# Optimization experiments

Hardware: AMD Instinct MI355X
Metric: run time of the kernel (lower is better)

## Reference

```python
import jax, jax.numpy as jnp
import numpy as np

B, F, P, DM = 1, 16, 256, 1024            # batch, frames, patches, mm_hidden_size
HID = 4096                                 # config.hidden_size
DI, DSTATE, DTRANK, DCONV = 2 * DM, 16, DM // 16, 4


def _layernorm(x, w, b):
    mu = x.mean(-1, keepdims=True)
    var = ((x - mu) ** 2).mean(-1, keepdims=True)
    return (x - mu) * jax.lax.rsqrt(var + 1e-5) * w + b


def _selective_scan(u, dt, A, Bm, Cm, Dv):
    # u, dt: [b,L,d]; Bm, Cm: [b,L,n]; A: [d,n]; Dv: [d]
    def step(h, inp):
        dt_t, B_t, C_t, u_t = inp  # [b,d],[b,n],[b,n],[b,d]
        h = jnp.exp(dt_t[..., None] * A) * h + (dt_t * u_t)[..., None] * B_t[:, None, :]
        return h, jnp.einsum('bdn,bn->bd', h, C_t)
    h0 = jnp.zeros((u.shape[0], A.shape[0], A.shape[1]), u.dtype)
    _, ys = jax.lax.scan(step, h0, (jnp.swapaxes(dt, 0, 1), jnp.swapaxes(Bm, 0, 1),
                                    jnp.swapaxes(Cm, 0, 1), jnp.swapaxes(u, 0, 1)))
    return jnp.swapaxes(ys, 0, 1) + u * Dv


def _mamba_block(x, ln_w, ln_b, in_proj_w, conv_w, conv_b, x_proj_w,
                 dt_proj_w, dt_proj_b, A_log, D_param, out_proj_w):
    res = x
    x = _layernorm(x, ln_w, ln_b)
    xz = x @ in_proj_w                       # [b,L,2*DI]
    xin, z = jnp.split(xz, 2, axis=-1)
    xt = jnp.swapaxes(xin, 1, 2)             # [b,DI,L]
    xt = jax.lax.conv_general_dilated(xt, conv_w[:, None, :], (1,), [(DCONV - 1, 0)],
                                      dimension_numbers=('NCH', 'OIH', 'NCH'),
                                      feature_group_count=DI)
    xt = xt + conv_b[:, None]
    u = jax.nn.silu(jnp.swapaxes(xt, 1, 2))  # [b,L,DI]
    x_dbl = u @ x_proj_w                     # [b,L,DTRANK+2*DSTATE]
    dt_raw, Bm, Cm = jnp.split(x_dbl, [DTRANK, DTRANK + DSTATE], axis=-1)
    dt = jax.nn.softplus(dt_raw @ dt_proj_w + dt_proj_b)
    A = -jnp.exp(A_log)
    y = _selective_scan(u, dt, A, Bm, Cm, D_param)
    y = y * jax.nn.silu(z)
    return res + y @ out_proj_w


def setup_inputs() -> dict:
    key = jax.random.key(0)
    ks = jax.random.split(key, 8)
    s = 0.02
    return {
        'vst': jax.random.normal(ks[0], (B, F, P, DM), jnp.float32),
        'ln_w': jnp.ones((DM,), jnp.float32), 'ln_b': jnp.zeros((DM,), jnp.float32),
        'in_proj_w': jax.random.normal(ks[1], (DM, 2 * DI), jnp.float32) * s,
        'conv_w': jax.random.normal(ks[2], (DI, DCONV), jnp.float32) * s,
        'conv_b': jnp.zeros((DI,), jnp.float32),
        'x_proj_w': jax.random.normal(ks[3], (DI, DTRANK + 2 * DSTATE), jnp.float32) * s,
        'dt_proj_w': jax.random.normal(ks[4], (DTRANK, DI), jnp.float32) * s,
        'dt_proj_b': jnp.full((DI,), -4.6, jnp.float32),  # softplus ~ 0.01
        'A_log': jnp.log(jnp.tile(jnp.arange(1, DSTATE + 1, dtype=jnp.float32), (DI, 1))),
        'D_param': jnp.ones((DI,), jnp.float32),
        'out_proj_w': jax.random.normal(ks[5], (DI, DM), jnp.float32) * s,
        'fln_w': jnp.ones((DM,), jnp.float32), 'fln_b': jnp.zeros((DM,), jnp.float32),
        'mlp_w1': jax.random.normal(ks[6], (DM, HID), jnp.float32) * s,
        'mlp_b1': jnp.zeros((HID,), jnp.float32),
        'mlp_w2': jax.random.normal(ks[7], (HID, HID), jnp.float32) * s,
        'mlp_b2': jnp.zeros((HID,), jnp.float32),
    }


def reference(vst, ln_w, ln_b, in_proj_w, conv_w, conv_b, x_proj_w, dt_proj_w,
              dt_proj_b, A_log, D_param, out_proj_w, fln_w, fln_b,
              mlp_w1, mlp_b1, mlp_w2, mlp_b2):
    b, f, p, d = vst.shape
    h = w = int(p ** 0.5)
    # the chain of rearranges in the source is a net reshape to b (f h w) d
    x = vst.reshape(b, f * h * w, d)
    x = _mamba_block(x, ln_w, ln_b, in_proj_w, conv_w, conv_b, x_proj_w,
                     dt_proj_w, dt_proj_b, A_log, D_param, out_proj_w)
    x = _layernorm(x, fln_w, fln_b)
    # AvgPool3d kernel=(1,4,4), stride=(1,4,4) over (f,h,w)
    x = x.reshape(b, f, h // 4, 4, w // 4, 4, d).mean(axis=(3, 5))
    x = x.reshape(b, f * (h // 4) * (w // 4), d)
    y = jax.nn.gelu(x @ mlp_w1 + mlp_b1, approximate=False)
    return y @ mlp_w2 + mlp_b2
```

## Files before the change

### kernel.cpp

```cpp
#include <hip/hip_runtime.h>
#include <hip/hip_bf16.h>
#include <math.h>

typedef __hip_bfloat16 bf16_t;
typedef __attribute__((ext_vector_type(8))) short short8;
typedef __attribute__((ext_vector_type(4))) float f32x4;

#define L_SEQ   4096
#define DMODEL  1024
#define DI      2048
#define NST     16
#define DTRANK  64
#define XDBL_N  96
#define HID     4096
#define CHUNK   32
#define NCHUNK  128
#define POOLED_ROWS 256

__device__ __forceinline__ void async_load16(const bf16_t* g, bf16_t* l) {
    __builtin_amdgcn_global_load_lds(
        (const __attribute__((address_space(1))) void*)g,
        (__attribute__((address_space(3))) void*)l,
        16, 0, 0);
}
__device__ __forceinline__ void async_load16f(const float* g, float* l) {
    __builtin_amdgcn_global_load_lds(
        (const __attribute__((address_space(1))) void*)g,
        (__attribute__((address_space(3))) void*)l,
        16, 0, 0);
}

__device__ __forceinline__ float softplus_f(float x) {
    return fmaxf(x, 0.f) + __logf(1.f + __expf(-fabsf(x)));
}

__global__ __launch_bounds__(256)
void transpose_all_kernel(const float* __restrict__ j0, bf16_t* __restrict__ o0,
                          const float* __restrict__ j1, bf16_t* __restrict__ o1,
                          const float* __restrict__ j2, bf16_t* __restrict__ o2,
                          const float* __restrict__ j3, bf16_t* __restrict__ o3,
                          const float* __restrict__ j4, bf16_t* __restrict__ o4) {
    int b = blockIdx.x;
    const float* in; bf16_t* out; int K, N, Npad, local;
    if (b < 512)        { in = j0; out = o0; K = 1024; N = 4096; Npad = 4096; local = b; }
    else if (b < 544)   { in = j1; out = o1; K = 2048; N = 96;   Npad = 128;  local = b - 512; }
    else if (b < 576)   { in = j2; out = o2; K = 64;   N = 2048; Npad = 2048; local = b - 544; }
    else if (b < 832)   { in = j3; out = o3; K = 2048; N = 1024; Npad = 1024; local = b - 576; }
    else                { in = j4; out = o4; K = 1024; N = 4096; Npad = 4096; local = b - 832; }
    int nt = Npad >> 6;
    int k0 = (local / nt) << 7, n0 = (local % nt) << 6;

    __shared__ float t[64 * 129];
    int tid = threadIdx.x;
    int kkb = tid >> 4;
    int nq  = (tid & 15) * 4;
#pragma unroll
    for (int it = 0; it < 8; it++) {
        int kl = it * 16 + kkb;
        int gk = k0 + kl, gn = n0 + nq;
        float4 v = {0.f, 0.f, 0.f, 0.f};
        if (gk < K) {
            const float* src = in + (size_t)gk * N + gn;
            if (gn + 3 < N) v = *(const float4*)src;
            else {
                if (gn + 0 < N) v.x = src[0];
                if (gn + 1 < N) v.y = src[1];
                if (gn + 2 < N) v.z = src[2];
                if (gn + 3 < N) v.w = src[3];
            }
        }
        t[(nq + 0) * 129 + kl] = v.x;
        t[(nq + 1) * 129 + kl] = v.y;
        t[(nq + 2) * 129 + kl] = v.z;
        t[(nq + 3) * 129 + kl] = v.w;
    }
    __syncthreads();
#pragma unroll
    for (int it = 0; it < 4; it++) {
        int slot = it * 256 + tid;
        int nn = slot >> 4, kc = (slot & 15) * 8;
        if (k0 + kc >= K) continue;
        const float* r = &t[nn * 129 + kc];
        short8 o;
#pragma unroll
        for (int j = 0; j < 8; j++) {
            bf16_t h = __float2bfloat16(r[j]);
            o[j] = *(short*)&h;
        }
        *(short8*)(out + (size_t)(n0 + nn) * K + k0 + kc) = o;
    }
}

__global__ __launch_bounds__(256)
void ln_kernel(const float* __restrict__ x, const float* __restrict__ w,
               const float* __restrict__ b, bf16_t* __restrict__ out) {
    int row = blockIdx.x;
    int tid = threadIdx.x;
    const float* xr = x + (size_t)row * DMODEL;
    float v[4];
    float s = 0.f, ss = 0.f;
#pragma unroll
    for (int e = 0; e < 4; e++) {
        v[e] = xr[tid + e * 256];
        s += v[e];
        ss += v[e] * v[e];
    }
#pragma unroll
    for (int off = 32; off > 0; off >>= 1) {
        s  += __shfl_down(s, off);
        ss += __shfl_down(ss, off);
    }
    __shared__ float rs[4], rss[4];
    int wid = tid >> 6;
    if ((tid & 63) == 0) { rs[wid] = s; rss[wid] = ss; }
    __syncthreads();
    s  = rs[0] + rs[1] + rs[2] + rs[3];
    ss = rss[0] + rss[1] + rss[2] + rss[3];
    float mu  = s * (1.f / DMODEL);
    float var = ss * (1.f / DMODEL) - mu * mu;
    float inv = rsqrtf(var + 1e-5f);
#pragma unroll
    for (int e = 0; e < 4; e++) {
        int col = tid + e * 256;
        out[(size_t)row * DMODEL + col] =
            __float2bfloat16((v[e] - mu) * inv * w[col] + b[col]);
    }
}

__global__ __launch_bounds__(256)
void ln_pool_a_kernel(const bf16_t* __restrict__ part, size_t pstride,
                      const float* __restrict__ res, const float* __restrict__ w,
                      const float* __restrict__ b, float* __restrict__ pool_part) {
    int blk = blockIdx.x;
    int p = blk >> 2, ii = blk & 3;
    int tid = threadIdx.x;
    int f = p >> 4, i4 = (p >> 2) & 3, j4 = p & 3;
    __shared__ float rs[4], rss[4];
    float acc[4] = {0.f, 0.f, 0.f, 0.f};
    float wv[4], bv[4];
#pragma unroll
    for (int e = 0; e < 4; e++) { wv[e] = w[tid + e * 256]; bv[e] = b[tid + e * 256]; }
    for (int jj = 0; jj < 4; jj++) {
        int row = f * 256 + (i4 * 4 + ii) * 16 + j4 * 4 + jj;
        size_t ro = (size_t)row * DMODEL;
        float v[4];
        float s = 0.f, ss = 0.f;
#pragma unroll
        for (int e = 0; e < 4; e++) {
            int col = tid + e * 256;
            float x = res[ro + col]
                    + __bfloat162float(part[ro + col])
                    + __bfloat162float(part[pstride + ro + col]);
            v[e] = x;
            s += x;
            ss += x * x;
        }
#pragma unroll
        for (int off = 32; off > 0; off >>= 1) {
            s  += __shfl_down(s, off);
            ss += __shfl_down(ss, off);
        }
        int wid = tid >> 6;
        if ((tid & 63) == 0) { rs[wid] = s; rss[wid] = ss; }
        __syncthreads();
        s  = rs[0] + rs[1] + rs[2] + rs[3];
        ss = rss[0] + rss[1] + rss[2] + rss[3];
        float mu  = s * (1.f / DMODEL);
        float var = ss * (1.f / DMODEL) - mu * mu;
        float inv = rsqrtf(var + 1e-5f);
#pragma unroll
        for (int e = 0; e < 4; e++)
            acc[e] += (v[e] - mu) * inv * wv[e] + bv[e];
        __syncthreads();
    }
#pragma unroll
    for (int e = 0; e < 4; e++)
        pool_part[(size_t)blk * DMODEL + tid + e * 256] = acc[e];
}

__global__ __launch_bounds__(256)
void ln_pool_b_kernel(const float* __restrict__ pool_part, bf16_t* __restrict__ pooled) {
    int idx = blockIdx.x * 256 + threadIdx.x;
    if (idx >= POOLED_ROWS * DMODEL) return;
    int p = idx >> 10, col = idx & (DMODEL - 1);
    float s = pool_part[(size_t)(p * 4 + 0) * DMODEL + col]
            + pool_part[(size_t)(p * 4 + 1) * DMODEL + col]
            + pool_part[(size_t)(p * 4 + 2) * DMODEL + col]
            + pool_part[(size_t)(p * 4 + 3) * DMODEL + col];
    pooled[idx] = __float2bfloat16(s * (1.f / 16.f));
}

template <int EPI>
__global__ __launch_bounds__(256, 2)
void mfma_gemm(const bf16_t* __restrict__ A, int lda,
               const bf16_t* __restrict__ Bt, int ldb,
               int K,
               float* __restrict__ Cf, bf16_t* __restrict__ Cb, int ldc,
               const float* __restrict__ bias, const float* __restrict__ res) {
    __shared__ bf16_t Asl[128 * 32];
    __shared__ bf16_t Bsl[128 * 32];
    const int tid = threadIdx.x;
    const int l = tid & 63, w = tid >> 6;
    const int m0 = blockIdx.y * 128, n0 = blockIdx.x * 128;
    const int wm = (w >> 1) * 64, wn = (w & 1) * 64;

    const int srow = tid >> 2;
    const int skc = (tid & 3) * 8;
    const bf16_t* Ag = A + (size_t)(m0 + srow) * lda + skc;
    const bf16_t* Bg = Bt + (size_t)(n0 + srow) * ldb + skc;
    bf16_t* As0 = Asl + (size_t)(w * 64) * 8;
    bf16_t* As1 = Asl + (size_t)(256 + w * 64) * 8;
    bf16_t* Bs0 = Bsl + (size_t)(w * 64) * 8;
    bf16_t* Bs1 = Bsl + (size_t)(256 + w * 64) * 8;

    f32x4 acc[4][4];
#pragma unroll
    for (int i = 0; i < 4; i++)
#pragma unroll
        for (int j = 0; j < 4; j++) acc[i][j] = (f32x4){0.f, 0.f, 0.f, 0.f};

    const short8* Asv = (const short8*)Asl;
    const short8* Bsv = (const short8*)Bsl;
    const int fr = l >> 4;
    const int fc = l & 15;

    for (int k0 = 0; k0 < K; k0 += 32) {
        __syncthreads();
        async_load16(Ag, As0);
        async_load16(Ag + (size_t)64 * lda, As1);
        async_load16(Bg, Bs0);
        async_load16(Bg + (size_t)64 * ldb, Bs1);
        Ag += 32; Bg += 32;
        __syncthreads();

        short8 a[4], b[4];
#pragma unroll
        for (int im = 0; im < 4; im++)
            a[im] = Asv[(wm + im * 16 + fc) * 4 + fr];
#pragma unroll
        for (int in = 0; in < 4; in++)
            b[in] = Bsv[(wn + in * 16 + fc) * 4 + fr];
#pragma unroll
        for (int im = 0; im < 4; im++)
#pragma unroll
            for (int in = 0; in < 4; in++)
                acc[im][in] = __builtin_amdgcn_mfma_f32_16x16x32_bf16(
                    a[im], b[in], acc[im][in], 0, 0, 0);
    }

#pragma unroll
    for (int im = 0; im < 4; im++) {
        int mbase = m0 + wm + im * 16 + fr * 4;
#pragma unroll
        for (int in = 0; in < 4; in++) {
            int n = n0 + wn + in * 16 + fc;
            float bv = (EPI == 1) ? bias[n] : 0.f;
#pragma unroll
            for (int v = 0; v < 4; v++) {
                float x = acc[im][in][v];
                size_t off = (size_t)(mbase + v) * ldc + n;
                if (EPI == 0) {
                    Cb[off] = __float2bfloat16(x);
                } else if (EPI == 1) {
                    Cb[off] = __float2bfloat16(softplus_f(x + bv));
                }
            }
        }
    }
}

template <bool PBF16>
__global__ __launch_bounds__(256, 2)
void mfma_gemm_splitk(const bf16_t* __restrict__ A, int lda,
                      const bf16_t* __restrict__ Bt, int ldb,
                      int Kper, void* __restrict__ Cpart, int ldc,
                      size_t pstride) {
    __shared__ bf16_t Asl[128 * 32];
    __shared__ bf16_t Bsl[128 * 32];
    const int tid = threadIdx.x;
    const int l = tid & 63, w = tid >> 6;
    const int m0 = blockIdx.y * 128, n0 = blockIdx.x * 128;
    const int wm = (w >> 1) * 64, wn = (w & 1) * 64;
    const int kbase = blockIdx.z * Kper;

    const int srow = tid >> 2;
    const int skc = (tid & 3) * 8;
    const bf16_t* Ag = A + (size_t)(m0 + srow) * lda + kbase + skc;
    const bf16_t* Bg = Bt + (size_t)(n0 + srow) * ldb + kbase + skc;
    bf16_t* As0 = Asl + (size_t)(w * 64) * 8;
    bf16_t* As1 = Asl + (size_t)(256 + w * 64) * 8;
    bf16_t* Bs0 = Bsl + (size_t)(w * 64) * 8;
    bf16_t* Bs1 = Bsl + (size_t)(256 + w * 64) * 8;

    f32x4 acc[4][4];
#pragma unroll
    for (int i = 0; i < 4; i++)
#pragma unroll
        for (int j = 0; j < 4; j++) acc[i][j] = (f32x4){0.f, 0.f, 0.f, 0.f};

    const short8* Asv = (const short8*)Asl;
    const short8* Bsv = (const short8*)Bsl;
    const int fr = l >> 4;
    const int fc = l & 15;

    for (int k0 = 0; k0 < Kper; k0 += 32) {
        __syncthreads();
        async_load16(Ag, As0);
        async_load16(Ag + (size_t)64 * lda, As1);
        async_load16(Bg, Bs0);
        async_load16(Bg + (size_t)64 * ldb, Bs1);
        Ag += 32; Bg += 32;
        __syncthreads();

        short8 a[4], b[4];
#pragma unroll
        for (int im = 0; im < 4; im++)
            a[im] = Asv[(wm + im * 16 + fc) * 4 + fr];
#pragma unroll
        for (int in = 0; in < 4; in++)
            b[in] = Bsv[(wn + in * 16 + fc) * 4 + fr];
#pragma unroll
        for (int im = 0; im < 4; im++)
#pragma unroll
            for (int in = 0; in < 4; in++)
                acc[im][in] = __builtin_amdgcn_mfma_f32_16x16x32_bf16(
                    a[im], b[in], acc[im][in], 0, 0, 0);
    }

#pragma unroll
    for (int im = 0; im < 4; im++) {
        int mbase = m0 + wm + im * 16 + fr * 4;
#pragma unroll
        for (int in = 0; in < 4; in++) {
            int n = n0 + wn + in * 16 + fc;
#pragma unroll
            for (int v = 0; v < 4; v++) {
                size_t o = (size_t)(mbase + v) * ldc + n;
                if (PBF16)
                    ((bf16_t*)Cpart)[(size_t)blockIdx.z * pstride + o] =
                        __float2bfloat16(acc[im][in][v]);
                else
                    ((float*)Cpart)[(size_t)blockIdx.z * pstride + o] = acc[im][in][v];
            }
        }
    }
}

__global__ __launch_bounds__(512, 1)
void gemm_nt_kernel(const bf16_t* __restrict__ A, int lda,
                    const float* __restrict__ B, int ldb,
                    int Kper, float* __restrict__ Cpart, int ldc,
                    size_t pstride) {
    __shared__ bf16_t Asl[256 * 32];
    __shared__ float  Bsl[32 * 64];
    const int tid = threadIdx.x;
    const int l = tid & 63, w = tid >> 6;
    const int n0 = blockIdx.x * 64;
    const int kbase = blockIdx.z * Kper;
    const int wm = w * 32;

    const int a_row = tid >> 2, a_kc = (tid & 3) * 8;
    const bf16_t* Ag = A + (size_t)a_row * lda + kbase + a_kc;
    bf16_t* As0 = Asl + (size_t)(w * 64) * 8;
    bf16_t* As1 = Asl + (size_t)(512 + w * 64) * 8;
    const int b_row = tid >> 4, b_nc = (tid & 15) * 4;
    const float* Bg = B + (size_t)(kbase + b_row) * ldb + n0 + b_nc;
    float* Bs0 = Bsl + (size_t)(w * 64) * 4;

    f32x4 acc[2][4];
#pragma unroll
    for (int i = 0; i < 2; i++)
#pragma unroll
        for (int j = 0; j < 4; j++) acc[i][j] = (f32x4){0.f, 0.f, 0.f, 0.f};

    const short8* Asv = (const short8*)Asl;
    const int fr = l >> 4, fc = l & 15;

    for (int k0 = 0; k0 < Kper; k0 += 32) {
        __syncthreads();
        async_load16(Ag, As0);
        async_load16(Ag + (size_t)128 * lda, As1);
        async_load16f(Bg, Bs0);
        Ag += 32;
        Bg += (size_t)32 * ldb;
        __syncthreads();

        short8 a[2], bfr[4];
        a[0] = Asv[(wm + fc) * 4 + fr];
        a[1] = Asv[(wm + 16 + fc) * 4 + fr];
#pragma unroll
        for (int j = 0; j < 4; j++) {
            const float* bp = Bsl + (size_t)(fr * 8) * 64 + j * 16 + fc;
            short8 t;
#pragma unroll
            for (int i = 0; i < 8; i++) {
                bf16_t h = __float2bfloat16(bp[i * 64]);
                t[i] = *(short*)&h;
            }
            bfr[j] = t;
        }
#pragma unroll
        for (int im = 0; im < 2; im++)
#pragma unroll
            for (int j = 0; j < 4; j++)
                acc[im][j] = __builtin_amdgcn_mfma_f32_16x16x32_bf16(
                    a[im], bfr[j], acc[im][j], 0, 0, 0);
    }

    float* Cz = Cpart + (size_t)blockIdx.z * pstride;
#pragma unroll
    for (int im = 0; im < 2; im++) {
        int mbase = wm + im * 16 + fr * 4;
#pragma unroll
        for (int j = 0; j < 4; j++) {
            int n = n0 + j * 16 + fc;
#pragma unroll
            for (int v = 0; v < 4; v++)
                Cz[(size_t)(mbase + v) * ldc + n] = acc[im][j][v];
        }
    }
}

template <int S, int EPI>
__global__ __launch_bounds__(256)
void reduce_splitk4(const float* __restrict__ part, size_t pstride, int ldp,
                    int M, int N, float* __restrict__ outf, bf16_t* __restrict__ outb,
                    int ldo, const float* __restrict__ bias) {
    int idx = blockIdx.x * 256 + threadIdx.x;
    int npr = N >> 2;
    if (idx >= M * npr) return;
    int r = idx / npr, c = (idx - r * npr) << 2;
    f32x4 s = (f32x4){0.f, 0.f, 0.f, 0.f};
#pragma unroll
    for (int z = 0; z < S; z++)
        s += *(const f32x4*)(part + (size_t)z * pstride + (size_t)r * ldp + c);
    size_t o = (size_t)r * ldo + c;
    if (EPI == 0) {
        *(f32x4*)(outf + o) = s;
        short8 pk;
        ushort4 ub;
#pragma unroll
        for (int e = 0; e < 4; e++) {
            bf16_t h = __float2bfloat16(s[e]);
            ((unsigned short*)&ub)[e] = *(unsigned short*)&h;
        }
        *(ushort4*)(outb + o) = ub;
        (void)pk;
    } else if (EPI == 1) {
        f32x4 bv = *(const f32x4*)(bias + c);
        ushort4 ub;
#pragma unroll
        for (int e = 0; e < 4; e++) {
            float x = s[e] + bv[e];
            x = 0.5f * x * (1.f + erff(x * 0.70710678118654752f));
            bf16_t h = __float2bfloat16(x);
            ((unsigned short*)&ub)[e] = *(unsigned short*)&h;
        }
        *(ushort4*)(outb + o) = ub;
    } else {
        f32x4 bv = *(const f32x4*)(bias + c);
        *(f32x4*)(outf + o) = s + bv;
    }
}

__global__ __launch_bounds__(256)
void conv_silu_kernel(const bf16_t* __restrict__ xz, const float* __restrict__ cw,
                      const float* __restrict__ cb, bf16_t* __restrict__ u) {
    int idx = blockIdx.x * 256 + threadIdx.x;
    if (idx >= L_SEQ * DI / 2) return;
    int chp = idx & (DI / 2 - 1);
    int l   = idx >> 10;
    int ch  = chp * 2;
    float acc0 = cb[ch], acc1 = cb[ch + 1];
    const float4* cwv = (const float4*)(cw + ch * 4);
    float4 c0 = cwv[0], c1 = cwv[1];
    float w0[4] = {c0.x, c0.y, c0.z, c0.w};
    float w1[4] = {c1.x, c1.y, c1.z, c1.w};
#pragma unroll
    for (int k = 0; k < 4; k++) {
        int ls = l - 3 + k;
        if (ls >= 0) {
            const bf16_t* p = xz + (size_t)ls * (2 * DI) + ch;
            acc0 += w0[k] * __bfloat162float(p[0]);
            acc1 += w1[k] * __bfloat162float(p[1]);
        }
    }
    float s0 = acc0 / (1.f + __expf(-acc0));
    float s1 = acc1 / (1.f + __expf(-acc1));
    bf16_t o0 = __float2bfloat16(s0), o1 = __float2bfloat16(s1);
    unsigned int packed = (unsigned int)*(unsigned short*)&o0 |
                          ((unsigned int)*(unsigned short*)&o1 << 16);
    *(unsigned int*)(u + (size_t)l * DI + ch) = packed;
}

__global__ __launch_bounds__(256)
void scan_pass1(const bf16_t* __restrict__ dt, const bf16_t* __restrict__ u,
                const float* __restrict__ x_dbl, const float* __restrict__ A_log,
                float* __restrict__ dtsum, float* __restrict__ Sw) {
    int c = blockIdx.x;
    int tid = threadIdx.x;
    int lane = tid & 63, w = tid >> 6;
    int dloc = w * 32 + (lane & 31);
    int n0 = (lane >> 5) * 8;
    int d = blockIdx.y * 128 + dloc;
    int l0 = c * CHUNK;
    __shared__ float sB[CHUNK * NST];
    for (int i = tid; i < CHUNK * NST; i += 256)
        sB[i] = x_dbl[(size_t)(l0 + (i >> 4)) * XDBL_N + DTRANK + (i & 15)];
    __syncthreads();
    float Areg[8], h[8];
#pragma unroll
    for (int j = 0; j < 8; j++) {
        Areg[j] = -__expf(A_log[d * NST + n0 + j]);
        h[j] = 0.f;
    }
    float dts = 0.f;
    float dtl = __bfloat162float(dt[(size_t)l0 * DI + d]);
    float ul  = __bfloat162float(u[(size_t)l0 * DI + d]);
    for (int l = 0; l < CHUNK; l++) {
        float dtn = 0.f, un = 0.f;
        if (l + 1 < CHUNK) {
            int gl = l0 + l + 1;
            dtn = __bfloat162float(dt[(size_t)gl * DI + d]);
            un  = __bfloat162float(u[(size_t)gl * DI + d]);
        }
        float du = dtl * ul;
        dts += dtl;
#pragma unroll
        for (int j = 0; j < 8; j++) {
            float a = __expf(dtl * Areg[j]);
            h[j] = a * h[j] + du * sB[l * NST + n0 + j];
        }
        dtl = dtn; ul = un;
    }
    size_t base = ((size_t)c * DI + d) * NST + n0;
#pragma unroll
    for (int j = 0; j < 8; j++)
        Sw[base + j] = h[j];
    if (n0 == 0)
        dtsum[(size_t)c * DI + d] = dts;
}

__global__ __launch_bounds__(256)
void scan_pass2(const float* __restrict__ dtsum, const float* __restrict__ A_log,
                float* __restrict__ SwInit) {
    int tid = blockIdx.x * 256 + threadIdx.x;
    if (tid >= DI * NST) return;
    int d = tid >> 4;
    float A = -__expf(A_log[tid]);
    const size_t DN = DI * NST;
    float h = 0.f;
    for (int c = 0; c < NCHUNK; c += 8) {
        float ds8[8], s8[8];
#pragma unroll
        for (int j = 0; j < 8; j++) {
            ds8[j] = dtsum[(size_t)(c + j) * DI + d];
            s8[j]  = SwInit[(size_t)(c + j) * DN + tid];
        }
#pragma unroll
        for (int j = 0; j < 8; j++) {
            float p = __expf(ds8[j] * A);
            SwInit[(size_t)(c + j) * DN + tid] = h;
            h = p * h + s8[j];
        }
    }
}

__global__ __launch_bounds__(256)
void scan_pass3(const bf16_t* __restrict__ dt, const bf16_t* __restrict__ u,
                const float* __restrict__ x_dbl, const float* __restrict__ A_log,
                const float* __restrict__ Dp, const float* __restrict__ initw,
                const bf16_t* __restrict__ xz, bf16_t* __restrict__ yy) {
    int c = blockIdx.x;
    int tid = threadIdx.x;
    int lane = tid & 63, w = tid >> 6;
    int dloc = w * 32 + (lane & 31);
    int n0 = (lane >> 5) * 8;
    int d = blockIdx.y * 128 + dloc;
    int l0 = c * CHUNK;
    __shared__ float sBC[CHUNK * 2 * NST];
    for (int i = tid; i < CHUNK * 2 * NST; i += 256)
        sBC[i] = x_dbl[(size_t)(l0 + (i >> 5)) * XDBL_N + DTRANK + (i & 31)];
    __syncthreads();
    float Areg[8], h[8];
    size_t base = ((size_t)c * DI + d) * NST + n0;
#pragma unroll
    for (int j = 0; j < 8; j++) {
        Areg[j] = -__expf(A_log[d * NST + n0 + j]);
        h[j] = initw[base + j];
    }
    float Dd = Dp[d];
    float dtl = __bfloat162float(dt[(size_t)l0 * DI + d]);
    float ul  = __bfloat162float(u[(size_t)l0 * DI + d]);
    float zv  = __bfloat162float(xz[(size_t)l0 * (2 * DI) + DI + d]);
    for (int l = 0; l < CHUNK; l++) {
        float dtn = 0.f, un = 0.f, zn = 0.f;
        if (l + 1 < CHUNK) {
            int gl = l0 + l + 1;
            dtn = __bfloat162float(dt[(size_t)gl * DI + d]);
            un  = __bfloat162float(u[(size_t)gl * DI + d]);
            zn  = __bfloat162float(xz[(size_t)gl * (2 * DI) + DI + d]);
        }
        float du = dtl * ul;
        float y = 0.f;
#pragma unroll
        for (int j = 0; j < 8; j++) {
            float a = __expf(dtl * Areg[j]);
            h[j] = a * h[j] + du * sBC[l * 32 + n0 + j];
            y += h[j] * sBC[l * 32 + NST + n0 + j];
        }
        y += __shfl_xor(y, 32);
        float sz = zv / (1.f + __expf(-zv));
        if ((lane >> 5) == 0)
            yy[(size_t)(l0 + l) * DI + d] = __float2bfloat16((y + ul * Dd) * sz);
        dtl = dtn; ul = un; zv = zn;
    }
}

extern "C" void kernel_launch(void* const* d_in, const int* in_sizes, int n_in,
                              void* d_out, int out_size, void* d_ws, size_t ws_size,
                              hipStream_t stream) {
    const float* vst        = (const float*)d_in[0];
    const float* ln_w       = (const float*)d_in[1];
    const float* ln_b       = (const float*)d_in[2];
    const float* in_proj_w  = (const float*)d_in[3];
    const float* conv_w     = (const float*)d_in[4];
    const float* conv_b     = (const float*)d_in[5];
    const float* x_proj_w   = (const float*)d_in[6];
    const float* dt_proj_w  = (const float*)d_in[7];
    const float* dt_proj_b  = (const float*)d_in[8];
    const float* A_log      = (const float*)d_in[9];
    const float* D_param    = (const float*)d_in[10];
    const float* out_proj_w = (const float*)d_in[11];
    const float* fln_w      = (const float*)d_in[12];
    const float* fln_b      = (const float*)d_in[13];
    const float* mlp_w1     = (const float*)d_in[14];
    const float* mlp_b1     = (const float*)d_in[15];
    const float* mlp_w2     = (const float*)d_in[16];
    const float* mlp_b2     = (const float*)d_in[17];
    float* out = (float*)d_out;

    char* wsb = (char*)d_ws;
    size_t off = 0;
    auto alloc_bf = [&](size_t n) { bf16_t* p = (bf16_t*)(wsb + off); off += n * 2; return p; };
    auto alloc_f  = [&](size_t n) { float*  p = (float*)(wsb + off); off += n * 4; return p; };

    bf16_t* w1t  = alloc_bf((size_t)(2 * DI) * DMODEL);
    bf16_t* xpt  = alloc_bf((size_t)128 * DI);
    bf16_t* dtpt = alloc_bf((size_t)DI * DTRANK);
    bf16_t* opt  = alloc_bf((size_t)DMODEL * DI);
    bf16_t* m1t  = alloc_bf((size_t)HID * DMODEL);
    bf16_t* m2t  = alloc_bf((size_t)HID * HID);
    bf16_t* xz_bf   = alloc_bf((size_t)L_SEQ * 2 * DI);
    bf16_t* u_bf    = alloc_bf((size_t)L_SEQ * DI);
    bf16_t* dt_bf   = alloc_bf((size_t)L_SEQ * DI);
    bf16_t* xdbl_bf = alloc_bf((size_t)L_SEQ * XDBL_N);
    bf16_t* yy_bf   = alloc_bf((size_t)L_SEQ * DI);
    float*  xdbl_f  = alloc_f((size_t)L_SEQ * XDBL_N);
    float*  Pw      = alloc_f((size_t)NCHUNK * DI * NST);
    float*  Sw      = alloc_f((size_t)NCHUNK * DI * NST);
    bf16_t* xn_bf   = yy_bf;
    float*  g2part  = Pw;
    float*  dtsum   = Pw;
    bf16_t* g4part  = xz_bf;
    bf16_t* pooled  = dt_bf;
    bf16_t* h1_bf   = dt_bf + (size_t)POOLED_ROWS * DMODEL;
    float*  pool_part = (float*)yy_bf;
    float*  g5part  = (float*)yy_bf;
    float*  g6part  = (float*)m2t;

    dim3 blk256(256);

    transpose_all_kernel<<<1344, blk256, 0, stream>>>(
        in_proj_w, w1t, x_proj_w, xpt, dt_proj_w, dtpt,
        out_proj_w, opt, mlp_w1, m1t);

    ln_kernel<<<L_SEQ, blk256, 0, stream>>>(vst, ln_w, ln_b, xn_bf);

    mfma_gemm<0><<<dim3((2 * DI) / 128, L_SEQ / 128), blk256, 0, stream>>>(
        xn_bf, DMODEL, w1t, DMODEL, DMODEL, nullptr, xz_bf, 2 * DI, nullptr, nullptr);

    conv_silu_kernel<<<(L_SEQ * DI / 2) / 256, blk256, 0, stream>>>(xz_bf, conv_w, conv_b, u_bf);

    mfma_gemm_splitk<false><<<dim3(1, L_SEQ / 128, 8), blk256, 0, stream>>>(
        u_bf, DI, xpt, DI, DI / 8, g2part, 128, (size_t)L_SEQ * 128);
    reduce_splitk4<8, 0><<<(L_SEQ * (XDBL_N / 4) + 255) / 256, blk256, 0, stream>>>(
        g2part, (size_t)L_SEQ * 128, 128, L_SEQ, XDBL_N, xdbl_f, xdbl_bf, XDBL_N, nullptr);

    mfma_gemm<1><<<dim3(DI / 128, L_SEQ / 128), blk256, 0, stream>>>(
        xdbl_bf, XDBL_N, dtpt, DTRANK, DTRANK, nullptr, dt_bf, DI, dt_proj_b, nullptr);

    scan_pass1<<<dim3(NCHUNK, DI / 128), blk256, 0, stream>>>(
        dt_bf, u_bf, xdbl_f, A_log, dtsum, Sw);
    scan_pass2<<<(DI * NST) / 256, blk256, 0, stream>>>(dtsum, A_log, Sw);
    scan_pass3<<<dim3(NCHUNK, DI / 128), blk256, 0, stream>>>(
        dt_bf, u_bf, xdbl_f, A_log, D_param, Sw, xz_bf, yy_bf);

    mfma_gemm_splitk<true><<<dim3(DMODEL / 128, L_SEQ / 128, 2), blk256, 0, stream>>>(
        yy_bf, DI, opt, DI, DI / 2, g4part, DMODEL, (size_t)L_SEQ * DMODEL);

    ln_pool_a_kernel<<<1024, blk256, 0, stream>>>(
        g4part, (size_t)L_SEQ * DMODEL, vst, fln_w, fln_b, pool_part);
    ln_pool_b_kernel<<<(POOLED_ROWS * DMODEL) / 256, blk256, 0, stream>>>(
        pool_part, pooled);

    mfma_gemm_splitk<false><<<dim3(HID / 128, POOLED_ROWS / 128, 4), blk256, 0, stream>>>(
        pooled, DMODEL, m1t, DMODEL, DMODEL / 4, g5part, HID, (size_t)POOLED_ROWS * HID);
    reduce_splitk4<4, 1><<<(POOLED_ROWS * (HID / 4)) / 256, blk256, 0, stream>>>(
        g5part, (size_t)POOLED_ROWS * HID, HID, POOLED_ROWS, HID, nullptr, h1_bf, HID, mlp_b1);

    gemm_nt_kernel<<<dim3(HID / 64, 1, 8), dim3(512), 0, stream>>>(
        h1_bf, HID, mlp_w2, HID, HID / 8, g6part, HID, (size_t)POOLED_ROWS * HID);
    reduce_splitk4<8, 2><<<(POOLED_ROWS * (HID / 4)) / 256, blk256, 0, stream>>>(
        g6part, (size_t)POOLED_ROWS * HID, HID, POOLED_ROWS, HID, out, nullptr, HID, mlp_b2);
}
```

Before: 435.3 us.

## Replace in_proj GEMM with 256x256 tile, 512-thread pipelined MFMA kernel

```diff
diff --git a/kernel.cpp b/kernel.cpp
--- a/kernel.cpp
+++ b/kernel.cpp
@@ -269,6 +269,140 @@
     }
 }
 
+__global__ __launch_bounds__(512, 2)
+void gemm_8ph_256(const bf16_t* __restrict__ A, int lda,
+                  const bf16_t* __restrict__ Bt, int ldb,
+                  int K, bf16_t* __restrict__ C, int ldc) {
+    __shared__ bf16_t Asm[2][2][128 * 64];
+    __shared__ bf16_t Bsm[2][2][128 * 64];
+
+    const int tid = threadIdx.x;
+    const int l   = tid & 63, wid = tid >> 6;
+    const int wm  = wid >> 2, wn = wid & 3;
+    const int fc  = l & 15, fr = l >> 4;
+
+    const int nwg  = gridDim.x * gridDim.y;
+    const int flat = blockIdx.y * gridDim.x + blockIdx.x;
+    const int swz  = (flat & 7) * (nwg >> 3) + (flat >> 3);
+    const int mt   = swz / gridDim.x;
+    const int nt   = swz - mt * gridDim.x;
+    const int m0 = mt * 256, n0 = nt * 256;
+
+    const int d0 = tid * 16;
+    const int s0 = d0 ^ (((d0 >> 9) & 1) << 5);
+    const int r0 = s0 >> 7;
+    const int c0 = (s0 & 127) >> 1;
+    const int wave64 = tid & ~63;
+
+    const bf16_t* Ag0 = A  + (size_t)(m0 + r0) * lda + c0;
+    const bf16_t* Ag1 = Ag0 + (size_t)128 * lda;
+    const bf16_t* Bg0 = Bt + (size_t)(n0 + r0) * ldb + c0;
+    const bf16_t* Bg1 = Bg0 + (size_t)128 * ldb;
+
+    auto stageA = [&](int buf, int half, int kt) {
+        const bf16_t* g = (half ? Ag1 : Ag0) + kt * 64;
+        bf16_t* dst = &Asm[buf][half][0] + wave64 * 8;
+        async_load16(g, dst);
+        async_load16(g + (size_t)64 * lda, dst + 4096);
+    };
+    auto stageB = [&](int buf, int half, int kt) {
+        const bf16_t* g = (half ? Bg1 : Bg0) + kt * 64;
+        bf16_t* dst = &Bsm[buf][half][0] + wave64 * 8;
+        async_load16(g, dst);
+        async_load16(g + (size_t)64 * ldb, dst + 4096);
+    };
+
+    const int laneOff = (fc * 128 + fr * 16) ^ ((fc & 4) << 3);
+
+    f32x4 acc[8][4];
+#pragma unroll
+    for (int i = 0; i < 8; i++)
+#pragma unroll
+        for (int j = 0; j < 4; j++) acc[i][j] = (f32x4){0.f, 0.f, 0.f, 0.f};
+
+    short8 a[2][2];
+    short8 b[4][2];
+
+#define BAR() __builtin_amdgcn_s_barrier()
+#define VMCNT6() do { asm volatile("s_waitcnt vmcnt(6)" ::: "memory"); \
+                      __builtin_amdgcn_sched_barrier(0); } while (0)
+#define RD_A(buf, q) do { \
+    const char* _ab = (const char*)&Asm[buf][wm][0] + (q) * 4096; \
+    a[0][0] = *(const short8*)(_ab + 0 + laneOff); \
+    a[0][1] = *(const short8*)(_ab + 64 + laneOff); \
+    a[1][0] = *(const short8*)(_ab + 2048 + laneOff); \
+    a[1][1] = *(const short8*)(_ab + 2048 + 64 + laneOff); \
+} while (0)
+#define RD_B(buf) do { \
+    const char* _bb = (const char*)&Bsm[buf][wn >> 1][0] + (wn & 1) * 8192; \
+    _Pragma("unroll") \
+    for (int _in = 0; _in < 4; _in++) { \
+        b[_in][0] = *(const short8*)(_bb + _in * 2048 + laneOff); \
+        b[_in][1] = *(const short8*)(_bb + _in * 2048 + 64 + laneOff); \
+    } \
+} while (0)
+#define MM(q) do { \
+    __builtin_amdgcn_s_setprio(1); \
+    _Pragma("unroll") \
+    for (int _ks = 0; _ks < 2; _ks++) \
+    _Pragma("unroll") \
+    for (int _in = 0; _in < 4; _in++) { \
+        acc[2*(q)][_in]   = __builtin_amdgcn_mfma_f32_16x16x32_bf16( \
+            a[0][_ks], b[_in][_ks], acc[2*(q)][_in], 0, 0, 0); \
+        acc[2*(q)+1][_in] = __builtin_amdgcn_mfma_f32_16x16x32_bf16( \
+            a[1][_ks], b[_in][_ks], acc[2*(q)+1][_in], 0, 0, 0); \
+    } \
+    __builtin_amdgcn_s_setprio(0); \
+} while (0)
+
+    const int NT = K >> 6;
+
+    stageA(0, 0, 0); stageB(0, 0, 0); stageA(0, 1, 0); stageB(0, 1, 0);
+    asm volatile("s_waitcnt vmcnt(4)" ::: "memory");
+    stageB(1, 0, 1); stageB(1, 1, 1); stageA(1, 0, 1);
+    asm volatile("s_waitcnt vmcnt(6)" ::: "memory");
+    __builtin_amdgcn_sched_barrier(0);
+    BAR();
+
+    for (int kt = 0; kt < NT; kt += 2) {
+        const int t2 = (kt + 2 < NT) ? kt + 2 : NT - 1;
+        const int t3 = (kt + 3 < NT) ? kt + 3 : NT - 1;
+        RD_B(0); RD_A(0, 0); stageA(1, 1, kt + 1);
+        BAR(); MM(0); BAR();
+        RD_A(0, 1); stageB(0, 0, t2);
+        BAR(); MM(1); BAR();
+        RD_A(0, 2); stageB(0, 1, t2);
+        BAR(); MM(2); BAR();
+        RD_A(0, 3); stageA(0, 0, t2);
+        BAR(); MM(3); VMCNT6(); BAR();
+        RD_B(1); RD_A(1, 0); stageA(0, 1, t2);
+        BAR(); MM(0); BAR();
+        RD_A(1, 1); stageB(1, 0, t3);
+        BAR(); MM(1); BAR();
+        RD_A(1, 2); stageB(1, 1, t3);
+        BAR(); MM(2); BAR();
+        RD_A(1, 3); stageA(1, 0, t3);
+        BAR(); MM(3); VMCNT6(); BAR();
+    }
+    asm volatile("s_waitcnt vmcnt(0)" ::: "memory");
+
+    bf16_t* Cp = C + (size_t)(m0 + wm * 128 + fr * 4) * ldc + n0 + wn * 64 + fc;
+#pragma unroll
+    for (int im = 0; im < 8; im++)
+#pragma unroll
+        for (int v = 0; v < 4; v++) {
+            bf16_t* row = Cp + (size_t)(im * 16 + v) * ldc;
+#pragma unroll
+            for (int in = 0; in < 4; in++)
+                row[in * 16] = __float2bfloat16(acc[im][in][v]);
+        }
+#undef BAR
+#undef VMCNT6
+#undef RD_A
+#undef RD_B
+#undef MM
+}
+
 template <bool PBF16>
 __global__ __launch_bounds__(256, 2)
 void mfma_gemm_splitk(const bf16_t* __restrict__ A, int lda,
@@ -437,7 +571,6 @@
     size_t o = (size_t)r * ldo + c;
     if (EPI == 0) {
         *(f32x4*)(outf + o) = s;
-        short8 pk;
         ushort4 ub;
 #pragma unroll
         for (int e = 0; e < 4; e++) {
@@ -445,7 +578,6 @@
             ((unsigned short*)&ub)[e] = *(unsigned short*)&h;
         }
         *(ushort4*)(outb + o) = ub;
-        (void)pk;
     } else if (EPI == 1) {
         f32x4 bv = *(const f32x4*)(bias + c);
         ushort4 ub;
@@ -677,8 +809,8 @@
 
     ln_kernel<<<L_SEQ, blk256, 0, stream>>>(vst, ln_w, ln_b, xn_bf);
 
-    mfma_gemm<0><<<dim3((2 * DI) / 128, L_SEQ / 128), blk256, 0, stream>>>(
-        xn_bf, DMODEL, w1t, DMODEL, DMODEL, nullptr, xz_bf, 2 * DI, nullptr, nullptr);
+    gemm_8ph_256<<<dim3((2 * DI) / 256, L_SEQ / 256), dim3(512), 0, stream>>>(
+        xn_bf, DMODEL, w1t, DMODEL, DMODEL, xz_bf, 2 * DI);
 
     conv_silu_kernel<<<(L_SEQ * DI / 2) / 256, blk256, 0, stream>>>(xz_bf, conv_w, conv_b, u_bf);
 
```

Result: no change. 430.2 us (-1.2%).
